# Performance work log

Hardware: AMD Instinct MI355X
Metric: run time of the kernel (lower is better)

Reference implementation:

```python
import jax, jax.numpy as jnp
import numpy as np

B, S, HID = 1, 2048, 2048
NH, NKV, HD = 32, 8, 64
INTER = 8192
EPS = 1e-6


def rmsnorm(x, w, eps=EPS):
    xf = x.astype(jnp.float32)
    inv = jax.lax.rsqrt(jnp.mean(xf * xf, axis=-1, keepdims=True) + eps)
    return (xf * inv * w).astype(x.dtype)


def rope(x, sin_t, cos_t):
    # x: [B, S, H, D]; sin/cos: [S, D//2]
    sin = sin_t[None, :, None, :]
    cos = cos_t[None, :, None, :]
    d2 = x.shape[-1] // 2
    x0, x1 = x[..., :d2], x[..., d2:]
    return jnp.concatenate((x0 * cos - x1 * sin, x0 * sin + x1 * cos), axis=-1)


def setup_inputs() -> dict:
    key = jax.random.key(0)
    ks = jax.random.split(key, 12)
    hidden_states = jax.random.normal(ks[0], (B, S, HID), dtype=jnp.float32)
    # realistic RoPE tables
    inv_freq = 1.0 / (10000.0 ** (np.arange(0, HD // 2, dtype=np.float32) * 2.0 / HD))
    ang = np.arange(S, dtype=np.float32)[:, None] * inv_freq[None, :]
    sin_table = jnp.asarray(np.sin(ang))
    cos_table = jnp.asarray(np.cos(ang))
    s = 0.02
    return {
        "hidden_states": hidden_states,
        "sin_table": sin_table,
        "cos_table": cos_table,
        "ln1_w": jnp.ones((HID,), jnp.float32),
        "ln2_w": jnp.ones((HID,), jnp.float32),
        "wq": jax.random.normal(ks[1], (HID, NH * HD), jnp.float32) * s,
        "wk": jax.random.normal(ks[2], (HID, NKV * HD), jnp.float32) * s,
        "wv": jax.random.normal(ks[3], (HID, NKV * HD), jnp.float32) * s,
        "wo": jax.random.normal(ks[4], (NH * HD, HID), jnp.float32) * s,
        "w_gate": jax.random.normal(ks[5], (HID, INTER), jnp.float32) * s,
        "w_up": jax.random.normal(ks[6], (HID, INTER), jnp.float32) * s,
        "w_down": jax.random.normal(ks[7], (INTER, HID), jnp.float32) * s,
    }


def attention(x, sin_t, cos_t, wq, wk, wv, wo):
    b, s, _ = x.shape
    q = (x @ wq).reshape(b, s, NH, HD)
    k = (x @ wk).reshape(b, s, NKV, HD)
    v = (x @ wv).reshape(b, s, NKV, HD).transpose(0, 2, 1, 3)  # [B,Hk,S,D]
    q = rope(q, sin_t, cos_t).transpose(0, 2, 1, 3)  # [B,Hq,S,D]
    k = rope(k, sin_t, cos_t).transpose(0, 2, 1, 3)  # [B,Hk,S,D]
    g = NH // NKV
    k = jnp.repeat(k, g, axis=1)
    v = jnp.repeat(v, g, axis=1)
    scale = 1.0 / np.sqrt(HD)
    scores = jnp.einsum("bhqd,bhkd->bhqk", q, k) * scale
    mask = jnp.tril(jnp.ones((s, s), dtype=bool))
    scores = jnp.where(mask, scores, -jnp.inf)
    probs = jax.nn.softmax(scores, axis=-1)
    out = jnp.einsum("bhqk,bhkd->bhqd", probs, v)
    out = out.transpose(0, 2, 1, 3).reshape(b, s, NH * HD)
    return out @ wo


def reference(hidden_states, sin_table, cos_table, ln1_w, ln2_w, wq, wk, wv, wo, w_gate, w_up, w_down):
    x = hidden_states
    x = x + attention(rmsnorm(x, ln1_w), sin_table, cos_table, wq, wk, wv, wo)
    h = rmsnorm(x, ln2_w)
    x = x + (jax.nn.silu(h @ w_gate) * (h @ w_up)) @ w_down
    return x
```

## Files before the change

kernel.cpp:

```cpp
#include <hip/hip_runtime.h>
#include <hip/hip_bf16.h>

typedef float f32x4 __attribute__((ext_vector_type(4)));
typedef unsigned int u32x4 __attribute__((ext_vector_type(4)));
typedef _Float16 f16x4 __attribute__((ext_vector_type(4)));
typedef unsigned short u16;

#define S_LEN 2048
#define HID 2048
#define NHEAD 32
#define NKVH 8
#define HDIM 64

__device__ __forceinline__ unsigned short f2bf_bits(float f) {
    unsigned int u = __builtin_bit_cast(unsigned int, f);
    unsigned int r = u + 0x7fffu + ((u >> 16) & 1u);
    return (unsigned short)(r >> 16);
}
__device__ __forceinline__ float bf2f(unsigned short b) {
    unsigned int u = ((unsigned int)b) << 16;
    return __builtin_bit_cast(float, u);
}

__device__ __forceinline__ f32x4 mfma_bf16(u32x4 a, u32x4 b, f32x4 c) {
    asm("v_mfma_f32_16x16x32_bf16 %0, %1, %2, %0" : "+v"(c) : "v"(a), "v"(b));
    return c;
}

__device__ __forceinline__ void gload_lds16(const void* g, void* l) {
    __builtin_amdgcn_global_load_lds(
        (const __attribute__((address_space(1))) void*)g,
        (__attribute__((address_space(3))) void*)l, 16, 0, 0);
}

__global__ __launch_bounds__(256)
void rmsnorm_k(const float* __restrict__ x, const float* __restrict__ wgt,
               unsigned short* __restrict__ out)
{
    int row = blockIdx.x;
    int t = threadIdx.x;
    const float* xr = x + (size_t)row * HID;
    f32x4 a = *(const f32x4*)(xr + t * 8);
    f32x4 b = *(const f32x4*)(xr + t * 8 + 4);
    float s = 0.f;
#pragma unroll
    for (int i = 0; i < 4; ++i) s += a[i] * a[i] + b[i] * b[i];
#pragma unroll
    for (int off = 32; off > 0; off >>= 1) s += __shfl_down(s, off);
    __shared__ float red[4];
    if ((t & 63) == 0) red[t >> 6] = s;
    __syncthreads();
    float tot = red[0] + red[1] + red[2] + red[3];
    float inv = rsqrtf(tot * (1.0f / (float)HID) + 1e-6f);
    f32x4 wa = *(const f32x4*)(wgt + t * 8);
    f32x4 wb = *(const f32x4*)(wgt + t * 8 + 4);
    unsigned int pk[4];
#pragma unroll
    for (int i = 0; i < 2; ++i) {
        pk[i]     = (unsigned)f2bf_bits(a[2*i] * inv * wa[2*i]) |
                    ((unsigned)f2bf_bits(a[2*i+1] * inv * wa[2*i+1]) << 16);
        pk[i + 2] = (unsigned)f2bf_bits(b[2*i] * inv * wb[2*i]) |
                    ((unsigned)f2bf_bits(b[2*i+1] * inv * wb[2*i+1]) << 16);
    }
    u32x4 ov; ov[0] = pk[0]; ov[1] = pk[1]; ov[2] = pk[2]; ov[3] = pk[3];
    *(u32x4*)(out + (size_t)row * HID + t * 8) = ov;
}

__global__ __launch_bounds__(256)
void transpose_cvt(const float* __restrict__ in, unsigned short* __restrict__ out,
                   int K, int N)
{
    __shared__ unsigned short tile[64 * 65];
    int kb = blockIdx.y * 64, nb = blockIdx.x * 64;
    int t = threadIdx.x;
    int r = t >> 2, c0 = (t & 3) * 16;
    const float* src = in + (size_t)(kb + r) * N + nb + c0;
#pragma unroll
    for (int j = 0; j < 4; ++j) {
        f32x4 v = *(const f32x4*)(src + j * 4);
#pragma unroll
        for (int i = 0; i < 4; ++i)
            tile[r * 65 + c0 + j * 4 + i] = f2bf_bits(v[i]);
    }
    __syncthreads();
    unsigned short e[16];
#pragma unroll
    for (int j = 0; j < 16; ++j) e[j] = tile[(c0 + j) * 65 + r];
    u32x4 o0, o1;
#pragma unroll
    for (int j = 0; j < 4; ++j) {
        o0[j] = (unsigned)e[2*j] | ((unsigned)e[2*j+1] << 16);
        o1[j] = (unsigned)e[8 + 2*j] | ((unsigned)e[8 + 2*j+1] << 16);
    }
    unsigned short* dst = out + (size_t)(nb + r) * K + kb + c0;
    *(u32x4*)(dst) = o0;
    *(u32x4*)(dst + 8) = o1;
}

__global__ __launch_bounds__(256)
void rope_k(unsigned short* __restrict__ qkv, const float* __restrict__ sin_t,
            const float* __restrict__ cos_t)
{
    int s = blockIdx.x;
    for (int it = threadIdx.x; it < (NHEAD + NKVH) * 32; it += 256) {
        int slot = it >> 5;
        int d = it & 31;
        int col = (slot < NHEAD) ? slot * 64 + d : HID + (slot - NHEAD) * 64 + d;
        unsigned short* p = qkv + (size_t)s * 3072 + col;
        float x0 = bf2f(p[0]);
        float x1 = bf2f(p[32]);
        float c = cos_t[s * 32 + d];
        float sn = sin_t[s * 32 + d];
        p[0]  = f2bf_bits(x0 * c - x1 * sn);
        p[32] = f2bf_bits(x0 * sn + x1 * c);
    }
}

__global__ __launch_bounds__(256)
void transpose_v(const unsigned short* __restrict__ qkv, unsigned short* __restrict__ vT)
{
    __shared__ unsigned short tile[64][80];
    int kb = blockIdx.x * 64, kvh = blockIdx.y;
    int t = threadIdx.x;
    int r = t >> 2, c0 = (t & 3) * 16;
    const unsigned short* src = qkv + (size_t)(kb + r) * 3072 + 2560 + kvh * 64 + c0;
    u32x4 v0 = *(const u32x4*)(src);
    u32x4 v1 = *(const u32x4*)(src + 8);
    *(u32x4*)&tile[r][c0] = v0;
    *(u32x4*)&tile[r][c0 + 8] = v1;
    __syncthreads();
    int d = t >> 2, k0 = (t & 3) * 16;
    unsigned short e[16];
#pragma unroll
    for (int j = 0; j < 16; ++j) e[j] = tile[k0 + j][d];
    u32x4 o0, o1;
#pragma unroll
    for (int j = 0; j < 4; ++j) {
        o0[j] = (unsigned)e[2*j] | ((unsigned)e[2*j+1] << 16);
        o1[j] = (unsigned)e[8 + 2*j] | ((unsigned)e[8 + 2*j+1] << 16);
    }
    int s0 = ((k0 >> 3) ^ (d & 7)) & 7;
    int s1 = (((k0 >> 3) + 1) ^ (d & 7)) & 7;
    unsigned short* dst = vT + ((size_t)kvh * 64 + d) * 2048 + kb;
    *(u32x4*)(dst + s0 * 8) = o0;
    *(u32x4*)(dst + s1 * 8) = o1;
}

template <int EPI>
__global__ __launch_bounds__(256)
void gemm_bt(const unsigned short* __restrict__ A,
             const unsigned short* __restrict__ Bt,
             void* __restrict__ outp, const void* __restrict__ auxp,
             int M, int N, int Kc, int lda)
{
    __shared__ unsigned short As[2][128 * 32];
    __shared__ unsigned short Bs[2][128 * 32];
    int t = threadIdx.x, w = t >> 6, l = t & 63;
    int rb = blockIdx.y, cb = blockIdx.x, zb = blockIdx.z;
    int wr = w >> 1, wc = w & 1;
    int l4 = l >> 4, l15 = l & 15;
    int arow = l >> 2, acol = (l & 3) * 8;
    f32x4 acc[4][4] = {};
    const unsigned short* Ag = A + (size_t)rb * 128 * lda + (size_t)zb * Kc
                                 + (size_t)(w * 16 + arow) * lda + acol;
    const unsigned short* Bg = Bt + (size_t)cb * 128 * lda + (size_t)zb * Kc
                                 + (size_t)(w * 16 + arow) * lda + acol;
    int nk = Kc >> 5;

#define STAGE(buf, kt)                                                          \
    {                                                                           \
        const unsigned short* Agk = Ag + (size_t)(kt) * 32;                     \
        const unsigned short* Bgk = Bg + (size_t)(kt) * 32;                     \
        gload_lds16(Agk, &As[buf][w * 512]);                                    \
        gload_lds16(Agk + (size_t)64 * lda, &As[buf][(4 + w) * 512]);           \
        gload_lds16(Bgk, &Bs[buf][w * 512]);                                    \
        gload_lds16(Bgk + (size_t)64 * lda, &Bs[buf][(4 + w) * 512]);           \
    }

    STAGE(0, 0);
    __syncthreads();
    int cur = 0;
    for (int kt = 0; kt < nk; ++kt) {
        if (kt + 1 < nk) STAGE(cur ^ 1, kt + 1);
        u32x4 af[4], bfr[4];
#pragma unroll
        for (int i = 0; i < 4; ++i)
            af[i] = *(const u32x4*)(&As[cur][(wr * 64 + i * 16 + l15) * 32 + l4 * 8]);
#pragma unroll
        for (int n = 0; n < 4; ++n)
            bfr[n] = *(const u32x4*)(&Bs[cur][(wc * 64 + n * 16 + l15) * 32 + l4 * 8]);
#pragma unroll
        for (int i = 0; i < 4; ++i)
#pragma unroll
            for (int n = 0; n < 4; ++n)
                acc[i][n] = mfma_bf16(af[i], bfr[n], acc[i][n]);
        __syncthreads();
        cur ^= 1;
    }
#undef STAGE

    int row0 = rb * 128 + wr * 64 + l4 * 4;
    int col0 = cb * 128 + wc * 64 + l15;
#pragma unroll
    for (int i = 0; i < 4; ++i) {
#pragma unroll
        for (int n = 0; n < 4; ++n) {
#pragma unroll
            for (int r = 0; r < 4; ++r) {
                int row = row0 + i * 16 + r;
                int col = col0 + n * 16;
                size_t idx = (size_t)row * N + col;
                float v = acc[i][n][r];
                if (EPI == 0) {
                    ((unsigned short*)outp)[idx] = f2bf_bits(v);
                } else if (EPI == 3) {
                    ((float*)outp)[idx] = v + ((const float*)auxp)[idx];
                } else {
                    ((_Float16*)outp)[(size_t)zb * M * N + idx] = (_Float16)v;
                }
            }
        }
    }
}

template <int KK, int QUAD, int WAITN>
__device__ __forceinline__ void phase8(u16* lds, int cur, f32x4 (&acc)[8][4],
                                       u32x4 (&bfv)[4],
                                       int aoff, int boff,
                                       const u16* Asrc, const u16* Bsrc,
                                       int lda, int kt_next, bool dostage,
                                       int dst0, int dst1)
{
    const u16* ah = lds + (cur * 4 + KK * 2) * 8192 + aoff + QUAD * 2048;
    u32x4 af[4];
#pragma unroll
    for (int mi = 0; mi < 4; ++mi) af[mi] = *(const u32x4*)(ah + mi * 512);
    if (QUAD == 0) {
        const u16* bh = lds + (cur * 4 + KK * 2 + 1) * 8192 + boff;
#pragma unroll
        for (int ni = 0; ni < 4; ++ni) bfv[ni] = *(const u32x4*)(bh + ni * 512);
    }
    if (dostage) {
        const u16* src = (QUAD ? Bsrc : Asrc) + (size_t)kt_next * 64 + KK * 32;
        u16* d = lds + ((cur ^ 1) * 4 + (KK * 2 + QUAD)) * 8192;
        gload_lds16(src, d + dst0);
        gload_lds16(src + (size_t)128 * lda, d + dst1);
    }
    __builtin_amdgcn_s_barrier();
    asm volatile("s_waitcnt lgkmcnt(0)" ::: "memory");
    __builtin_amdgcn_sched_barrier(0);
    __builtin_amdgcn_s_setprio(1);
#pragma unroll
    for (int mi = 0; mi < 4; ++mi)
#pragma unroll
        for (int ni = 0; ni < 4; ++ni)
            acc[QUAD * 4 + mi][ni] = mfma_bf16(af[mi], bfv[ni], acc[QUAD * 4 + mi][ni]);
    __builtin_amdgcn_s_setprio(0);
    if (WAITN == 4) asm volatile("s_waitcnt vmcnt(4)" ::: "memory");
    else if (WAITN == 0) asm volatile("s_waitcnt vmcnt(0)" ::: "memory");
    __builtin_amdgcn_s_barrier();
}

template <int EPI>
__global__ __launch_bounds__(512, 2)
void gemm8p(const u16* __restrict__ A, const u16* __restrict__ Bt,
            void* __restrict__ outp, const void* __restrict__ auxp,
            int M, int N, int Kc, int lda)
{
    extern __shared__ u16 lds[];
    const int tid = threadIdx.x;
    const int w = tid >> 6, l = tid & 63;
    const int wm = w >> 2, wn = w & 3;
    const int l4 = l >> 4, l15 = l & 15;
    const int zb = blockIdx.y;

    int wg = blockIdx.x, nwg = gridDim.x;
    int swzb = ((nwg & 7) == 0) ? ((wg & 7) * (nwg >> 3) + (wg >> 3)) : wg;
    int rbs = M >> 8;
    int rb = swzb % rbs, cb = swzb / rbs;

    const int sw = ((tid & 3) ^ ((tid >> 3) & 3)) * 8;
    const int srow = tid >> 2;
    const u16* Asrc = A + (size_t)(rb * 256 + srow) * lda + (size_t)zb * Kc + sw;
    const u16* Bsrc = Bt + (size_t)(cb * 256 + srow) * lda + (size_t)zb * Kc + sw;
    const int dst0 = tid * 8, dst1 = (512 + tid) * 8;

    const int rswz = (l15 >> 1) & 3;
    const int aoff = (wm * 128 + l15) * 32 + (l4 ^ rswz) * 8;
    const int boff = (wn * 64 + l15) * 32 + (l4 ^ rswz) * 8;

    f32x4 acc[8][4] = {};
    u32x4 bfv[4];
    const int NT = Kc >> 6;

#pragma unroll
    for (int h = 0; h < 2; ++h) {
        const u16* sA = Asrc + h * 32;
        const u16* sB = Bsrc + h * 32;
        gload_lds16(sA, lds + (h * 2) * 8192 + dst0);
        gload_lds16(sA + (size_t)128 * lda, lds + (h * 2) * 8192 + dst1);
        gload_lds16(sB, lds + (h * 2 + 1) * 8192 + dst0);
        gload_lds16(sB + (size_t)128 * lda, lds + (h * 2 + 1) * 8192 + dst1);
    }
    asm volatile("s_waitcnt vmcnt(4)" ::: "memory");
    __builtin_amdgcn_s_barrier();

    for (int t = 0; t < NT - 1; ++t) {
        int cur = t & 1;
        phase8<0, 0, -1>(lds, cur, acc, bfv, aoff, boff, Asrc, Bsrc, lda, t + 1, true, dst0, dst1);
        phase8<0, 1,  4>(lds, cur, acc, bfv, aoff, boff, Asrc, Bsrc, lda, t + 1, true, dst0, dst1);
        phase8<1, 0, -1>(lds, cur, acc, bfv, aoff, boff, Asrc, Bsrc, lda, t + 1, true, dst0, dst1);
        phase8<1, 1,  4>(lds, cur, acc, bfv, aoff, boff, Asrc, Bsrc, lda, t + 1, true, dst0, dst1);
    }
    {
        int cur = (NT - 1) & 1;
        phase8<0, 0, -1>(lds, cur, acc, bfv, aoff, boff, Asrc, Bsrc, lda, 0, false, dst0, dst1);
        phase8<0, 1,  0>(lds, cur, acc, bfv, aoff, boff, Asrc, Bsrc, lda, 0, false, dst0, dst1);
        phase8<1, 0, -1>(lds, cur, acc, bfv, aoff, boff, Asrc, Bsrc, lda, 0, false, dst0, dst1);
        phase8<1, 1, -1>(lds, cur, acc, bfv, aoff, boff, Asrc, Bsrc, lda, 0, false, dst0, dst1);
    }

    int row0 = rb * 256 + wm * 128 + l4 * 4;
    int col0 = cb * 256 + wn * 64 + l15;
#pragma unroll
    for (int mi = 0; mi < 8; ++mi) {
#pragma unroll
        for (int ni = 0; ni < 4; ++ni) {
#pragma unroll
            for (int r = 0; r < 4; ++r) {
                int row = row0 + mi * 16 + r;
                int col = col0 + ni * 16;
                size_t idx = (size_t)row * N + col;
                float v = acc[mi][ni][r];
                if (EPI == 1) {
                    float sv = v / (1.0f + __expf(-v));
                    ((unsigned short*)outp)[idx] = f2bf_bits(sv);
                } else if (EPI == 2) {
                    float gv = bf2f(((const unsigned short*)auxp)[idx]);
                    ((unsigned short*)outp)[idx] = f2bf_bits(v * gv);
                } else {
                    ((_Float16*)outp)[(size_t)zb * M * N + idx] = (_Float16)v;
                }
            }
        }
    }
}

__global__ __launch_bounds__(256)
void reduce_add4(float* __restrict__ out, const _Float16* __restrict__ p, int n)
{
    int i = (blockIdx.x * 256 + threadIdx.x) * 4;
    f32x4 a = *(const f32x4*)(out + i);
#pragma unroll
    for (int z = 0; z < 4; ++z) {
        f16x4 h = *(const f16x4*)(p + (size_t)z * n + i);
#pragma unroll
        for (int j = 0; j < 4; ++j) a[j] += (float)h[j];
    }
    *(f32x4*)(out + i) = a;
}

__global__ __launch_bounds__(256)
void reduce_res2(float* __restrict__ out, const float* __restrict__ x,
                 const _Float16* __restrict__ p, int n)
{
    int i = (blockIdx.x * 256 + threadIdx.x) * 4;
    f32x4 a = *(const f32x4*)(x + i);
#pragma unroll
    for (int z = 0; z < 2; ++z) {
        f16x4 h = *(const f16x4*)(p + (size_t)z * n + i);
#pragma unroll
        for (int j = 0; j < 4; ++j) a[j] += (float)h[j];
    }
    *(f32x4*)(out + i) = a;
}

__global__ __launch_bounds__(256)
void attn_fwd(const unsigned short* __restrict__ qkv,
              const unsigned short* __restrict__ vT,
              unsigned short* __restrict__ out)
{
    int p = blockIdx.x, h = blockIdx.y, kvh = h >> 2;
    int t = threadIdx.x, w = t >> 6, l = t & 63;
    int l4 = l >> 4, l15 = l & 15;
    __shared__ unsigned short Ks[2][64 * 64];
    __shared__ unsigned short Vs[2][64 * 64];
    __shared__ unsigned short Pl[4][16 * 72];
    unsigned short* Pw = &Pl[w][0];

    const unsigned short* Kg = qkv + HID + kvh * 64;
    const unsigned short* Vg = vT + (size_t)kvh * 64 * 2048;

    int ch0 = w * 2, ch1 = w * 2 + 1;
    int rsub = l >> 3;
    int ksw = ((l & 7) ^ (rsub & 7)) * 8;
    int vcol = (l & 7) * 8;
    int sw0 = (l4 ^ (l15 & 7)) * 8;
    int sw1 = ((l4 | 4) ^ (l15 & 7)) * 8;

#define STAGE_KV(buf, kt)                                                         \
    {                                                                             \
        gload_lds16(Kg + (size_t)((kt) * 64 + ch0 * 8 + rsub) * 3072 + ksw,       \
                    &Ks[buf][ch0 * 512]);                                         \
        gload_lds16(Kg + (size_t)((kt) * 64 + ch1 * 8 + rsub) * 3072 + ksw,       \
                    &Ks[buf][ch1 * 512]);                                         \
        gload_lds16(Vg + (size_t)(ch0 * 8 + rsub) * 2048 + (kt) * 64 + vcol,      \
                    &Vs[buf][ch0 * 512]);                                         \
        gload_lds16(Vg + (size_t)(ch1 * 8 + rsub) * 2048 + (kt) * 64 + vcol,      \
                    &Vs[buf][ch1 * 512]);                                         \
    }

    const float SC2 = 0.18033688f;
    const float THR = 44.36f;
    const float BIG = -3.0e38f;

    for (int half = 0; half < 2; ++half) {
        int qb = half ? (31 - p) : p;
        int qrow0 = qb * 64 + w * 16;
        STAGE_KV(0, 0);
        const unsigned short* qg = qkv + (size_t)(qrow0 + l15) * 3072 + h * 64 + l4 * 8;
        u32x4 aq0 = *(const u32x4*)(qg);
        u32x4 aq1 = *(const u32x4*)(qg + 32);
        f32x4 o[4] = {};
        float m[4], ls[4] = {};
#pragma unroll
        for (int r = 0; r < 4; ++r) m[r] = BIG;
        __syncthreads();
        int cur = 0;
        for (int kt = 0; kt <= qb; ++kt) {
            if (kt < qb) STAGE_KV(cur ^ 1, kt + 1);
            f32x4 sc[4];
#pragma unroll
            for (int n = 0; n < 4; ++n) {
                const unsigned short* kb_ = &Ks[cur][(n * 16 + l15) * 64];
                u32x4 b0 = *(const u32x4*)(kb_ + sw0);
                u32x4 b1 = *(const u32x4*)(kb_ + sw1);
                f32x4 z = {};
                z = mfma_bf16(aq0, b0, z);
                z = mfma_bf16(aq1, b1, z);
                sc[n] = z;
            }
            if (kt == qb) {
#pragma unroll
                for (int n = 0; n < 4; ++n) {
                    int kcol = n * 16 + l15;
#pragma unroll
                    for (int r = 0; r < 4; ++r) {
                        int qr = w * 16 + l4 * 4 + r;
                        if (kcol > qr) sc[n][r] = BIG;
                    }
                }
            }
            float rmax[4];
#pragma unroll
            for (int r = 0; r < 4; ++r)
                rmax[r] = fmaxf(fmaxf(sc[0][r], sc[1][r]), fmaxf(sc[2][r], sc[3][r]));
#pragma unroll
            for (int msk = 1; msk <= 8; msk <<= 1)
#pragma unroll
                for (int r = 0; r < 4; ++r)
                    rmax[r] = fmaxf(rmax[r], __shfl_xor(rmax[r], msk));
            float need = 0.f;
#pragma unroll
            for (int r = 0; r < 4; ++r) need = fmaxf(need, rmax[r] - m[r]);
            if (__ballot(need > THR)) {
#pragma unroll
                for (int r = 0; r < 4; ++r) {
                    float mn = fmaxf(m[r], rmax[r]);
                    float al = __builtin_exp2f((m[r] - mn) * SC2);
                    m[r] = mn;
                    ls[r] *= al;
#pragma unroll
                    for (int nd = 0; nd < 4; ++nd) o[nd][r] *= al;
                }
            }
            float rs[4] = {}, ms[4];
#pragma unroll
            for (int r = 0; r < 4; ++r) ms[r] = m[r] * SC2;
#pragma unroll
            for (int n = 0; n < 4; ++n)
#pragma unroll
                for (int r = 0; r < 4; ++r) {
                    float pe = __builtin_exp2f(__builtin_fmaf(sc[n][r], SC2, -ms[r]));
                    sc[n][r] = pe;
                    rs[r] += pe;
                }
#pragma unroll
            for (int msk = 1; msk <= 8; msk <<= 1)
#pragma unroll
                for (int r = 0; r < 4; ++r) rs[r] += __shfl_xor(rs[r], msk);
#pragma unroll
            for (int r = 0; r < 4; ++r) ls[r] += rs[r];
#pragma unroll
            for (int n = 0; n < 4; ++n)
#pragma unroll
                for (int r = 0; r < 4; ++r)
                    Pw[(l4 * 4 + r) * 72 + n * 16 + l15] = f2bf_bits(sc[n][r]);
            asm volatile("s_waitcnt lgkmcnt(0)" ::: "memory");
            __builtin_amdgcn_sched_barrier(0);
            u32x4 ap0 = *(const u32x4*)(Pw + l15 * 72 + l4 * 8);
            u32x4 ap1 = *(const u32x4*)(Pw + l15 * 72 + 32 + l4 * 8);
#pragma unroll
            for (int nd = 0; nd < 4; ++nd) {
                const unsigned short* vb = &Vs[cur][(nd * 16 + l15) * 64];
                u32x4 bv0 = *(const u32x4*)(vb + sw0);
                u32x4 bv1 = *(const u32x4*)(vb + sw1);
                o[nd] = mfma_bf16(ap0, bv0, o[nd]);
                o[nd] = mfma_bf16(ap1, bv1, o[nd]);
            }
            __syncthreads();
            cur ^= 1;
        }
#undef STAGE_KV
        float linv[4];
#pragma unroll
        for (int r = 0; r < 4; ++r) linv[r] = 1.0f / ls[r];
#pragma unroll
        for (int nd = 0; nd < 4; ++nd)
#pragma unroll
            for (int r = 0; r < 4; ++r)
                out[(size_t)(qrow0 + l4 * 4 + r) * HID + h * 64 + nd * 16 + l15] =
                    f2bf_bits(o[nd][r] * linv[r]);
    }
}

extern "C" void kernel_launch(void* const* d_in, const int* in_sizes, int n_in,
                              void* d_out, int out_size, void* d_ws, size_t ws_size,
                              hipStream_t stream)
{
    const float* x     = (const float*)d_in[0];
    const float* sin_t = (const float*)d_in[1];
    const float* cos_t = (const float*)d_in[2];
    const float* ln1w  = (const float*)d_in[3];
    const float* ln2w  = (const float*)d_in[4];
    const float* wq    = (const float*)d_in[5];
    const float* wk    = (const float*)d_in[6];
    const float* wv    = (const float*)d_in[7];
    const float* wo    = (const float*)d_in[8];
    const float* wg    = (const float*)d_in[9];
    const float* wu    = (const float*)d_in[10];
    const float* wd    = (const float*)d_in[11];
    float* out = (float*)d_out;

    char* ws = (char*)d_ws;
    if (ws_size < 113246208u) return;
    unsigned short* wT   = (unsigned short*)(ws);
    unsigned short* xn   = (unsigned short*)(ws + 33554432u);
    unsigned short* qkv  = (unsigned short*)(ws + 41943040u);
    unsigned short* attn = (unsigned short*)(ws + 54525952u);
    unsigned short* vT   = (unsigned short*)(ws + 62914560u);
    _Float16*       part = (_Float16*)(ws + 33554432u);
    unsigned short* g    = (unsigned short*)(ws + 79691776u);
    _Float16*       opart = (_Float16*)(ws + 79691776u);

    hipFuncSetAttribute(reinterpret_cast<const void*>(&gemm8p<1>),
                        hipFuncAttributeMaxDynamicSharedMemorySize, 131072);
    hipFuncSetAttribute(reinterpret_cast<const void*>(&gemm8p<2>),
                        hipFuncAttributeMaxDynamicSharedMemorySize, 131072);
    hipFuncSetAttribute(reinterpret_cast<const void*>(&gemm8p<5>),
                        hipFuncAttributeMaxDynamicSharedMemorySize, 131072);

    rmsnorm_k<<<S_LEN, 256, 0, stream>>>(x, ln1w, xn);

    transpose_cvt<<<dim3(32, 32), 256, 0, stream>>>(wq, wT, 2048, 2048);
    transpose_cvt<<<dim3(8, 32), 256, 0, stream>>>(wk, wT + (size_t)2048 * 2048, 2048, 512);
    transpose_cvt<<<dim3(8, 32), 256, 0, stream>>>(wv, wT + (size_t)2560 * 2048, 2048, 512);

    gemm_bt<0><<<dim3(24, 16, 1), 256, 0, stream>>>(xn, wT, qkv, nullptr, 2048, 3072, 2048, 2048);

    rope_k<<<S_LEN, 256, 0, stream>>>(qkv, sin_t, cos_t);
    transpose_v<<<dim3(32, 8), 256, 0, stream>>>(qkv, vT);

    attn_fwd<<<dim3(16, 32), 256, 0, stream>>>(qkv, vT, attn);

    transpose_cvt<<<dim3(32, 32), 256, 0, stream>>>(wo, wT, 2048, 2048);
    gemm_bt<5><<<dim3(16, 16, 2), 256, 0, stream>>>(attn, wT, opart, nullptr, 2048, 2048, 1024, 2048);
    reduce_res2<<<4096, 256, 0, stream>>>(out, x, opart, 4194304);

    rmsnorm_k<<<S_LEN, 256, 0, stream>>>(out, ln2w, xn);

    transpose_cvt<<<dim3(128, 32), 256, 0, stream>>>(wg, wT, 2048, 8192);
    gemm8p<1><<<dim3(256, 1), 512, 131072, stream>>>(xn, wT, g, nullptr, 2048, 8192, 2048, 2048);

    transpose_cvt<<<dim3(128, 32), 256, 0, stream>>>(wu, wT, 2048, 8192);
    gemm8p<2><<<dim3(256, 1), 512, 131072, stream>>>(xn, wT, g, g, 2048, 8192, 2048, 2048);

    transpose_cvt<<<dim3(32, 128), 256, 0, stream>>>(wd, wT, 8192, 2048);
    gemm8p<5><<<dim3(64, 4), 512, 131072, stream>>>(g, wT, part, nullptr, 2048, 2048, 2048, 8192);

    reduce_add4<<<4096, 256, 0, stream>>>(out, part, 4194304);
}
```

Before: 465.3 us.

## Transpose attention MFMA operands to keep P in registers, drop LDS round-trip

The attention kernel now swaps the MFMA operands so each lane holds a single query row's scores. Row max and sum then reduce with two cross-lane shuffles instead of four per row, and the softmax state becomes a scalar per lane. The P tile is packed to bf16 with v_cvt_pk_bf16 and redistributed to the PV MFMA operand layout through lane shuffles, replacing the LDS store, wait and reload. The output store becomes a packed 8-byte write. The shuffle-based redistribution costs extra ds_bpermute operations in exchange for removing the LDS P buffer.

```diff
diff --git a/kernel.cpp b/kernel.cpp
--- a/kernel.cpp
+++ b/kernel.cpp
@@ -3,6 +3,7 @@
 
 typedef float f32x4 __attribute__((ext_vector_type(4)));
 typedef unsigned int u32x4 __attribute__((ext_vector_type(4)));
+typedef unsigned int u32x2 __attribute__((ext_vector_type(2)));
 typedef _Float16 f16x4 __attribute__((ext_vector_type(4)));
 typedef unsigned short u16;
 
@@ -20,6 +21,11 @@
 __device__ __forceinline__ float bf2f(unsigned short b) {
     unsigned int u = ((unsigned int)b) << 16;
     return __builtin_bit_cast(float, u);
+}
+__device__ __forceinline__ unsigned cvt_pk_bf16(float lo, float hi) {
+    unsigned d;
+    asm("v_cvt_pk_bf16_f32 %0, %1, %2" : "=v"(d) : "v"(lo), "v"(hi));
+    return d;
 }
 
 __device__ __forceinline__ f32x4 mfma_bf16(u32x4 a, u32x4 b, f32x4 c) {
@@ -385,8 +391,6 @@
     int l4 = l >> 4, l15 = l & 15;
     __shared__ unsigned short Ks[2][64 * 64];
     __shared__ unsigned short Vs[2][64 * 64];
-    __shared__ unsigned short Pl[4][16 * 72];
-    unsigned short* Pw = &Pl[w][0];
 
     const unsigned short* Kg = qkv + HID + kvh * 64;
     const unsigned short* Vg = vT + (size_t)kvh * 64 * 2048;
@@ -397,6 +401,9 @@
     int vcol = (l & 7) * 8;
     int sw0 = (l4 ^ (l15 & 7)) * 8;
     int sw1 = ((l4 | 4) ^ (l15 & 7)) * 8;
+    int srcA = ((l >> 4) & 1) * 32 + l15;
+    int srcB = srcA + 16;
+    bool hi32 = (l & 32) != 0;
 
 #define STAGE_KV(buf, kt)                                                         \
     {                                                                             \
@@ -422,9 +429,7 @@
         u32x4 aq0 = *(const u32x4*)(qg);
         u32x4 aq1 = *(const u32x4*)(qg + 32);
         f32x4 o[4] = {};
-        float m[4], ls[4] = {};
-#pragma unroll
-        for (int r = 0; r < 4; ++r) m[r] = BIG;
+        float m = BIG, ls = 0.f;
         __syncthreads();
         int cur = 0;
         for (int kt = 0; kt <= qb; ++kt) {
@@ -436,91 +441,88 @@
                 u32x4 b0 = *(const u32x4*)(kb_ + sw0);
                 u32x4 b1 = *(const u32x4*)(kb_ + sw1);
                 f32x4 z = {};
-                z = mfma_bf16(aq0, b0, z);
-                z = mfma_bf16(aq1, b1, z);
+                z = mfma_bf16(b0, aq0, z);
+                z = mfma_bf16(b1, aq1, z);
                 sc[n] = z;
             }
             if (kt == qb) {
-#pragma unroll
-                for (int n = 0; n < 4; ++n) {
-                    int kcol = n * 16 + l15;
-#pragma unroll
-                    for (int r = 0; r < 4; ++r) {
-                        int qr = w * 16 + l4 * 4 + r;
-                        if (kcol > qr) sc[n][r] = BIG;
-                    }
+                int qloc = w * 16 + l15;
+#pragma unroll
+                for (int n = 0; n < 4; ++n)
+#pragma unroll
+                    for (int r = 0; r < 4; ++r)
+                        if (n * 16 + l4 * 4 + r > qloc) sc[n][r] = BIG;
+            }
+            float rmax = BIG;
+#pragma unroll
+            for (int n = 0; n < 4; ++n)
+#pragma unroll
+                for (int r = 0; r < 4; ++r) rmax = fmaxf(rmax, sc[n][r]);
+            rmax = fmaxf(rmax, __shfl_xor(rmax, 16));
+            rmax = fmaxf(rmax, __shfl_xor(rmax, 32));
+            if (__ballot(rmax - m > THR)) {
+                float mn = fmaxf(m, rmax);
+                float al = __builtin_exp2f((m - mn) * SC2);
+                m = mn;
+                ls *= al;
+#pragma unroll
+                for (int nd = 0; nd < 4; ++nd)
+#pragma unroll
+                    for (int r = 0; r < 4; ++r) o[nd][r] *= al;
+            }
+            float ms = m * SC2, rs = 0.f;
+#pragma unroll
+            for (int n = 0; n < 4; ++n)
+#pragma unroll
+                for (int r = 0; r < 4; ++r) {
+                    float pe = __builtin_exp2f(__builtin_fmaf(sc[n][r], SC2, -ms));
+                    sc[n][r] = pe;
+                    rs += pe;
                 }
-            }
-            float rmax[4];
-#pragma unroll
-            for (int r = 0; r < 4; ++r)
-                rmax[r] = fmaxf(fmaxf(sc[0][r], sc[1][r]), fmaxf(sc[2][r], sc[3][r]));
-#pragma unroll
-            for (int msk = 1; msk <= 8; msk <<= 1)
-#pragma unroll
-                for (int r = 0; r < 4; ++r)
-                    rmax[r] = fmaxf(rmax[r], __shfl_xor(rmax[r], msk));
-            float need = 0.f;
-#pragma unroll
-            for (int r = 0; r < 4; ++r) need = fmaxf(need, rmax[r] - m[r]);
-            if (__ballot(need > THR)) {
-#pragma unroll
-                for (int r = 0; r < 4; ++r) {
-                    float mn = fmaxf(m[r], rmax[r]);
-                    float al = __builtin_exp2f((m[r] - mn) * SC2);
-                    m[r] = mn;
-                    ls[r] *= al;
-#pragma unroll
-                    for (int nd = 0; nd < 4; ++nd) o[nd][r] *= al;
-                }
-            }
-            float rs[4] = {}, ms[4];
-#pragma unroll
-            for (int r = 0; r < 4; ++r) ms[r] = m[r] * SC2;
-#pragma unroll
-            for (int n = 0; n < 4; ++n)
-#pragma unroll
-                for (int r = 0; r < 4; ++r) {
-                    float pe = __builtin_exp2f(__builtin_fmaf(sc[n][r], SC2, -ms[r]));
-                    sc[n][r] = pe;
-                    rs[r] += pe;
-                }
-#pragma unroll
-            for (int msk = 1; msk <= 8; msk <<= 1)
-#pragma unroll
-                for (int r = 0; r < 4; ++r) rs[r] += __shfl_xor(rs[r], msk);
-#pragma unroll
-            for (int r = 0; r < 4; ++r) ls[r] += rs[r];
-#pragma unroll
-            for (int n = 0; n < 4; ++n)
-#pragma unroll
-                for (int r = 0; r < 4; ++r)
-                    Pw[(l4 * 4 + r) * 72 + n * 16 + l15] = f2bf_bits(sc[n][r]);
-            asm volatile("s_waitcnt lgkmcnt(0)" ::: "memory");
-            __builtin_amdgcn_sched_barrier(0);
-            u32x4 ap0 = *(const u32x4*)(Pw + l15 * 72 + l4 * 8);
-            u32x4 ap1 = *(const u32x4*)(Pw + l15 * 72 + 32 + l4 * 8);
+            rs += __shfl_xor(rs, 16);
+            rs += __shfl_xor(rs, 32);
+            ls += rs;
+            unsigned pk0[2], pk1[2], pk2[2], pk3[2];
+#pragma unroll
+            for (int rr = 0; rr < 2; ++rr) {
+                pk0[rr] = cvt_pk_bf16(sc[0][2*rr], sc[0][2*rr+1]);
+                pk1[rr] = cvt_pk_bf16(sc[1][2*rr], sc[1][2*rr+1]);
+                pk2[rr] = cvt_pk_bf16(sc[2][2*rr], sc[2][2*rr+1]);
+                pk3[rr] = cvt_pk_bf16(sc[3][2*rr], sc[3][2*rr+1]);
+            }
+            u32x4 W1, W2;
+            {
+                unsigned a0, a1;
+                a0 = __shfl(pk0[0], srcA); a1 = __shfl(pk1[0], srcA); W1[0] = hi32 ? a1 : a0;
+                a0 = __shfl(pk0[1], srcA); a1 = __shfl(pk1[1], srcA); W1[1] = hi32 ? a1 : a0;
+                a0 = __shfl(pk0[0], srcB); a1 = __shfl(pk1[0], srcB); W1[2] = hi32 ? a1 : a0;
+                a0 = __shfl(pk0[1], srcB); a1 = __shfl(pk1[1], srcB); W1[3] = hi32 ? a1 : a0;
+                a0 = __shfl(pk2[0], srcA); a1 = __shfl(pk3[0], srcA); W2[0] = hi32 ? a1 : a0;
+                a0 = __shfl(pk2[1], srcA); a1 = __shfl(pk3[1], srcA); W2[1] = hi32 ? a1 : a0;
+                a0 = __shfl(pk2[0], srcB); a1 = __shfl(pk3[0], srcB); W2[2] = hi32 ? a1 : a0;
+                a0 = __shfl(pk2[1], srcB); a1 = __shfl(pk3[1], srcB); W2[3] = hi32 ? a1 : a0;
+            }
 #pragma unroll
             for (int nd = 0; nd < 4; ++nd) {
                 const unsigned short* vb = &Vs[cur][(nd * 16 + l15) * 64];
                 u32x4 bv0 = *(const u32x4*)(vb + sw0);
                 u32x4 bv1 = *(const u32x4*)(vb + sw1);
-                o[nd] = mfma_bf16(ap0, bv0, o[nd]);
-                o[nd] = mfma_bf16(ap1, bv1, o[nd]);
+                o[nd] = mfma_bf16(bv0, W1, o[nd]);
+                o[nd] = mfma_bf16(bv1, W2, o[nd]);
             }
             __syncthreads();
             cur ^= 1;
         }
 #undef STAGE_KV
-        float linv[4];
-#pragma unroll
-        for (int r = 0; r < 4; ++r) linv[r] = 1.0f / ls[r];
-#pragma unroll
-        for (int nd = 0; nd < 4; ++nd)
-#pragma unroll
-            for (int r = 0; r < 4; ++r)
-                out[(size_t)(qrow0 + l4 * 4 + r) * HID + h * 64 + nd * 16 + l15] =
-                    f2bf_bits(o[nd][r] * linv[r]);
+        float linv = 1.0f / ls;
+        unsigned short* orow = out + (size_t)(qrow0 + l15) * HID + h * 64 + l4 * 4;
+#pragma unroll
+        for (int nd = 0; nd < 4; ++nd) {
+            u32x2 wv;
+            wv[0] = cvt_pk_bf16(o[nd][0] * linv, o[nd][1] * linv);
+            wv[1] = cvt_pk_bf16(o[nd][2] * linv, o[nd][3] * linv);
+            *(u32x2*)(orow + nd * 16) = wv;
+        }
     }
 }
 
```

Result: faster. 450.4 us (-3.2%).
